# Kernel optimization log

Measured on AMD Instinct MI355X. Metric: run time of the kernel, lower is better.

## Reference

```python
import jax, jax.numpy as jnp
import numpy as np

K, B, D, H = 8, 8192, 1024, 256


def setup_inputs() -> dict:
    key = jax.random.key(0)
    k_x, k_w1, k_w2 = jax.random.split(key, 3)
    x = jax.random.normal(k_x, (B, D), dtype=jnp.float32)
    # He-ish scaled weights so reconstructions stay finite
    W1 = jax.random.normal(k_w1, (K, D, H), dtype=jnp.float32) * (1.0 / np.sqrt(D))
    b1 = jnp.zeros((K, H), dtype=jnp.float32)
    W2 = jax.random.normal(k_w2, (K, H, D), dtype=jnp.float32) * (1.0 / np.sqrt(H))
    b2 = jnp.zeros((K, D), dtype=jnp.float32)
    return {"x": x, "W1": W1, "b1": b1, "W2": W2, "b2": b2}


def reference(x, W1, b1, W2, b2):
    # Run every expert AE on the full batch (matches predict()):
    h = jax.nn.relu(jnp.einsum('bd,kdh->kbh', x, W1) + b1[:, None, :])   # [K,B,H]
    recon = jnp.einsum('kbh,khd->kbd', h, W2) + b2[:, None, :]            # [K,B,D]
    # per-sample reconstruction MSE per expert
    err = jnp.mean((recon - x[None]) ** 2, axis=-1)                       # [K,B]
    # cluster_assignment = argmax over (-err) == argmin over err
    assign = jnp.argmin(err, axis=0)                                      # [B] int
    # gather-compute-scatter: select the winning expert's reconstruction
    x_out = recon[assign, jnp.arange(recon.shape[1])]                     # [B,D]
    return x_out
```

## Files before the change

### kernel.cpp

```cpp
#include <hip/hip_runtime.h>


#define KE 8
#define NB 8192
#define ND 1024
#define NH 256

typedef float f32x4 __attribute__((ext_vector_type(4)));
typedef short s16x8 __attribute__((ext_vector_type(8)));
typedef unsigned short u16x8 __attribute__((ext_vector_type(8)));

__device__ __forceinline__ float bf2f(unsigned short h) {
  union { unsigned int u; float f; } v; v.u = ((unsigned int)h) << 16; return v.f;
}
__device__ __forceinline__ unsigned short f2bf(float f) {
  union { unsigned int u; float f; } v; v.f = f;
  unsigned int u = v.u;
  u += 0x7fffu + ((u >> 16) & 1u);
  return (unsigned short)(u >> 16);
}
__device__ __forceinline__ void split2(float x, unsigned short& hi, unsigned short& lo) {
  hi = f2bf(x);
  lo = f2bf(x - bf2f(hi));
}

__global__ __launch_bounds__(256) void pack_all(
    const float* __restrict__ W1, unsigned short* __restrict__ w1oh, unsigned short* __restrict__ w1ol,
    const float* __restrict__ W2, unsigned short* __restrict__ w2oh, unsigned short* __restrict__ w2ol,
    const float* __restrict__ xin, unsigned short* __restrict__ xoh, unsigned short* __restrict__ xol,
    unsigned int* __restrict__ cnt) {
  const int bx = blockIdx.x;
  const int tid = threadIdx.x;
  if (bx == 0 && tid < KE) cnt[tid] = 0;

  if (bx < 1024) {
    int gid = bx * 256 + tid;
    int L = gid & 63;
    int g = gid >> 6;
    int ks = g & 31;
    int ct = (g >> 5) & 15;
    int k = g >> 9;
    int col = ct * 16 + (L & 15);
    int kd0 = ks * 32 + (L >> 4) * 8;
    unsigned short th[8], tl[8];
#pragma unroll
    for (int j = 0; j < 8; ++j) {
      float v = W1[((size_t)k * ND + kd0 + j) * NH + col];
      split2(v, th[j], tl[j]);
    }
    size_t o = ((size_t)g * 64 + L) * 8;
    *(u16x8*)&w1oh[o] = *(u16x8*)th;
    *(u16x8*)&w1ol[o] = *(u16x8*)tl;
  } else if (bx < 2048) {
    int gid = (bx - 1024) * 256 + tid;
    int L = gid & 63;
    int g = gid >> 6;
    int ks = g & 7;
    int dt = (g >> 3) & 63;
    int k = g >> 9;
    int d2 = dt * 16 + (L & 15);
    int h0 = ks * 32 + (L >> 4) * 8;
    unsigned short th[8], tl[8];
#pragma unroll
    for (int j = 0; j < 8; ++j) {
      float v = W2[((size_t)k * NH + h0 + j) * ND + d2];
      split2(v, th[j], tl[j]);
    }
    size_t o = ((size_t)g * 64 + L) * 8;
    *(u16x8*)&w2oh[o] = *(u16x8*)th;
    *(u16x8*)&w2ol[o] = *(u16x8*)tl;
  } else {
    int gid = (bx - 2048) * 256 + tid;
    int L = gid & 63;
    int g = gid >> 6;
    int ks = g & 31;
    int rt = g >> 5;
    int row = rt * 16 + (L & 15);
    int kd0 = ks * 32 + (L >> 4) * 8;
    float4 a = *(const float4*)&xin[(size_t)row * ND + kd0];
    float4 b = *(const float4*)&xin[(size_t)row * ND + kd0 + 4];
    unsigned short th[8], tl[8];
    split2(a.x, th[0], tl[0]); split2(a.y, th[1], tl[1]);
    split2(a.z, th[2], tl[2]); split2(a.w, th[3], tl[3]);
    split2(b.x, th[4], tl[4]); split2(b.y, th[5], tl[5]);
    split2(b.z, th[6], tl[6]); split2(b.w, th[7], tl[7]);
    size_t o = ((size_t)g * 64 + L) * 8;
    *(u16x8*)&xoh[o] = *(u16x8*)th;
    *(u16x8*)&xol[o] = *(u16x8*)tl;
  }
}

#define LOAD_STAGE(ah, al, bh, bl, it)                  \
  do {                                                  \
    _Pragma("unroll")                                   \
    for (int q_ = 0; q_ < 4; ++q_) {                    \
      int o_ = xo[q_] + (it) * 512;                     \
      ah[q_] = *(const s16x8*)&xph[o_];                 \
      al[q_] = *(const s16x8*)&xpl[o_];                 \
    }                                                   \
    _Pragma("unroll")                                   \
    for (int q_ = 0; q_ < 4; ++q_) {                    \
      int o_ = wo1[q_] + (it) * 512;                    \
      bh[q_] = *(const s16x8*)&w1ph[o_];                \
      bl[q_] = *(const s16x8*)&w1pl[o_];                \
    }                                                   \
  } while (0)

#define MFMA_STAGE(ah, al, bh, bl)                                                                   \
  do {                                                                                               \
    _Pragma("unroll")                                                                                \
    for (int nt_ = 0; nt_ < 4; ++nt_)                                                                \
      _Pragma("unroll")                                                                              \
      for (int mt_ = 0; mt_ < 4; ++mt_) {                                                            \
        acc1[mt_][nt_] = __builtin_amdgcn_mfma_f32_16x16x32_bf16(ah[mt_], bh[nt_], acc1[mt_][nt_], 0, 0, 0); \
        acc1[mt_][nt_] = __builtin_amdgcn_mfma_f32_16x16x32_bf16(ah[mt_], bl[nt_], acc1[mt_][nt_], 0, 0, 0); \
        acc1[mt_][nt_] = __builtin_amdgcn_mfma_f32_16x16x32_bf16(al[mt_], bh[nt_], acc1[mt_][nt_], 0, 0, 0); \
      }                                                                                              \
  } while (0)

__global__ __launch_bounds__(256, 2) void ae_pass1(
    const unsigned short* __restrict__ xph, const unsigned short* __restrict__ xpl,
    const float* __restrict__ x,
    const unsigned short* __restrict__ w1ph, const unsigned short* __restrict__ w1pl,
    const float* __restrict__ b1,
    const unsigned short* __restrict__ w2ph, const unsigned short* __restrict__ w2pl,
    const float* __restrict__ b2, float* __restrict__ err) {
  __shared__ union {
    struct { unsigned short h[64][256]; unsigned short l[64][256]; } hs;
    float errp[4][64];
  } s;

  const int tid = threadIdx.x;
  const int wv = tid >> 6;
  const int lane = tid & 63;
  const int lo = lane & 15;
  const int quad = lane >> 4;
  const int k = (blockIdx.x >> 3) & 7;
  const int rtile = (int)(((blockIdx.x >> 6) << 3) | (blockIdx.x & 7));
  const int r0 = rtile * 64;

  int xo[4], wo1[4];
#pragma unroll
  for (int mt = 0; mt < 4; ++mt) xo[mt] = ((rtile * 4 + mt) * 32) * 512 + lane * 8;
#pragma unroll
  for (int nt = 0; nt < 4; ++nt) wo1[nt] = ((k * 16 + wv * 4 + nt) * 32) * 512 + lane * 8;

  f32x4 acc1[4][4];
#pragma unroll
  for (int mt = 0; mt < 4; ++mt)
#pragma unroll
    for (int nt = 0; nt < 4; ++nt) acc1[mt][nt] = (f32x4){0.f, 0.f, 0.f, 0.f};

  s16x8 Aah[4], Aal[4], Abh[4], Abl[4];
  s16x8 Bah[4], Bal[4], Bbh[4], Bbl[4];
  LOAD_STAGE(Aah, Aal, Abh, Abl, 0);
  LOAD_STAGE(Bah, Bal, Bbh, Bbl, 1);
  for (int it = 0; it < 32; it += 2) {
    MFMA_STAGE(Aah, Aal, Abh, Abl);
    if (it + 2 < 32) LOAD_STAGE(Aah, Aal, Abh, Abl, it + 2);
    MFMA_STAGE(Bah, Bal, Bbh, Bbl);
    if (it + 3 < 32) LOAD_STAGE(Bah, Bal, Bbh, Bbl, it + 3);
  }

#pragma unroll
  for (int nt = 0; nt < 4; ++nt) {
    float b1v = b1[(size_t)k * NH + wv * 64 + nt * 16 + lo];
#pragma unroll
    for (int mt = 0; mt < 4; ++mt)
#pragma unroll
      for (int i = 0; i < 4; ++i) {
        float v = acc1[mt][nt][i] + b1v;
        v = v > 0.f ? v : 0.f;
        unsigned short vh, vl;
        split2(v, vh, vl);
        int row = mt * 16 + quad * 4 + i, col = wv * 64 + nt * 16 + lo;
        int sc = col ^ ((row & 7) << 3);
        s.hs.h[row][sc] = vh;
        s.hs.l[row][sc] = vl;
      }
  }
  __syncthreads();

  float eacc[4][4];
#pragma unroll
  for (int mt = 0; mt < 4; ++mt)
#pragma unroll
    for (int i = 0; i < 4; ++i) eacc[mt][i] = 0.f;

  const int w2base = ((k * 64 + wv * 16) * 8) * 512 + lane * 8;

  for (int mc = 0; mc < 2; ++mc) {
    s16x8 hh[2][8], hl[2][8];
#pragma unroll
    for (int m2 = 0; m2 < 2; ++m2) {
      int row = (mc * 2 + m2) * 16 + lo;
      int rbase = row * 256;
      int sw = (row & 7) << 3;
#pragma unroll
      for (int ks = 0; ks < 8; ++ks) {
        int off = rbase + ((ks * 32 + quad * 8) ^ sw);
        hh[m2][ks] = *(const s16x8*)(&s.hs.h[0][0] + off);
        hl[m2][ks] = *(const s16x8*)(&s.hs.l[0][0] + off);
      }
    }
    for (int dt = 0; dt < 16; ++dt) {
      f32x4 acc2[2];
      acc2[0] = (f32x4){0.f, 0.f, 0.f, 0.f};
      acc2[1] = (f32x4){0.f, 0.f, 0.f, 0.f};
#pragma unroll
      for (int ks = 0; ks < 8; ++ks) {
        int wo = w2base + dt * 4096 + ks * 512;
        s16x8 bh = *(const s16x8*)&w2ph[wo];
        s16x8 bl = *(const s16x8*)&w2pl[wo];
#pragma unroll
        for (int m2 = 0; m2 < 2; ++m2) {
          acc2[m2] = __builtin_amdgcn_mfma_f32_16x16x32_bf16(hh[m2][ks], bh, acc2[m2], 0, 0, 0);
          acc2[m2] = __builtin_amdgcn_mfma_f32_16x16x32_bf16(hh[m2][ks], bl, acc2[m2], 0, 0, 0);
          acc2[m2] = __builtin_amdgcn_mfma_f32_16x16x32_bf16(hl[m2][ks], bh, acc2[m2], 0, 0, 0);
        }
      }
      const int d2 = wv * 256 + dt * 16 + lo;
      float b2v = b2[(size_t)k * ND + d2];
#pragma unroll
      for (int m2 = 0; m2 < 2; ++m2)
#pragma unroll
        for (int i = 0; i < 4; ++i) {
          int row = (mc * 2 + m2) * 16 + quad * 4 + i;
          float rec = acc2[m2][i] + b2v;
          float xv = x[(size_t)(r0 + row) * ND + d2];
          float dd = rec - xv;
          eacc[mc * 2 + m2][i] += dd * dd;
        }
    }
  }

  __syncthreads();
#pragma unroll
  for (int mt = 0; mt < 4; ++mt)
#pragma unroll
    for (int i = 0; i < 4; ++i) {
      float v = eacc[mt][i];
      v += __shfl_xor(v, 1, 16);
      v += __shfl_xor(v, 2, 16);
      v += __shfl_xor(v, 4, 16);
      v += __shfl_xor(v, 8, 16);
      if (lo == 0) s.errp[wv][mt * 16 + quad * 4 + i] = v;
    }
  __syncthreads();
  if (tid < 64)
    err[(size_t)k * NB + r0 + tid] =
        (s.errp[0][tid] + s.errp[1][tid] + s.errp[2][tid] + s.errp[3][tid]) * (1.0f / (float)ND);
}

__global__ __launch_bounds__(256) void ae_argmin(const float* __restrict__ err,
                                                 unsigned int* __restrict__ cnt,
                                                 int* __restrict__ bucket) {
  __shared__ unsigned int lc[KE];
  __shared__ unsigned int base[KE];
  int tid = threadIdx.x;
  if (tid < KE) lc[tid] = 0;
  __syncthreads();
  int b = blockIdx.x * 256 + tid;
  float best = err[b];
  int kmin = 0;
#pragma unroll
  for (int j = 1; j < KE; ++j) {
    float e = err[(size_t)j * NB + b];
    if (e < best) { best = e; kmin = j; }
  }
  unsigned int lpos = atomicAdd(&lc[kmin], 1u);
  __syncthreads();
  if (tid < KE) base[tid] = atomicAdd(&cnt[tid], lc[tid]);
  __syncthreads();
  bucket[(size_t)kmin * NB + (int)(base[kmin] + lpos)] = b;
}

__global__ __launch_bounds__(256) void ae_pass2(
    const float* __restrict__ x,
    const unsigned short* __restrict__ w1ph, const float* __restrict__ b1,
    const unsigned short* __restrict__ w2ph, const float* __restrict__ b2,
    const unsigned int* __restrict__ cnt, const int* __restrict__ bucket,
    float* __restrict__ out) {
  __shared__ unsigned short hs[64][NH + 8];
  __shared__ unsigned short xs[64][40];
  __shared__ int rid[64];

  const int k = blockIdx.x & 7;
  const int cv = (int)cnt[k];
  const int t0 = (blockIdx.x >> 3) * 64;
  if (t0 >= cv) return;
  const int nrows = min(64, cv - t0);

  const int tid = threadIdx.x;
  const int wv = tid >> 6;
  const int lane = tid & 63;
  const int lo = lane & 15;
  const int quad = lane >> 4;
  const int srow = tid >> 2, scol = (tid & 3) * 8;

  if (tid < 64) {
    int idx = t0 + tid;
    rid[tid] = bucket[(size_t)k * NB + (idx < cv ? idx : t0)];
  }
  __syncthreads();
  const int grow = rid[srow];

  f32x4 acc1[4][4];
#pragma unroll
  for (int mt = 0; mt < 4; ++mt)
#pragma unroll
    for (int nt = 0; nt < 4; ++nt) acc1[mt][nt] = (f32x4){0.f, 0.f, 0.f, 0.f};

  for (int it = 0; it < 32; ++it) {
    float4 xa = *(const float4*)&x[(size_t)grow * ND + it * 32 + scol];
    float4 xb = *(const float4*)&x[(size_t)grow * ND + it * 32 + scol + 4];
    s16x8 bfr[4];
#pragma unroll
    for (int nt = 0; nt < 4; ++nt)
      bfr[nt] = *(const s16x8*)&w1ph[(((size_t)(k * 16 + wv * 4 + nt) * 32) + it) * 512 + lane * 8];
    __syncthreads();
    unsigned short t[8];
    t[0] = f2bf(xa.x); t[1] = f2bf(xa.y); t[2] = f2bf(xa.z); t[3] = f2bf(xa.w);
    t[4] = f2bf(xb.x); t[5] = f2bf(xb.y); t[6] = f2bf(xb.z); t[7] = f2bf(xb.w);
    *(u16x8*)&xs[srow][scol] = *(u16x8*)t;
    __syncthreads();
    s16x8 af[4];
#pragma unroll
    for (int mt = 0; mt < 4; ++mt) af[mt] = *(const s16x8*)&xs[mt * 16 + lo][quad * 8];
#pragma unroll
    for (int mt = 0; mt < 4; ++mt)
#pragma unroll
      for (int nt = 0; nt < 4; ++nt)
        acc1[mt][nt] = __builtin_amdgcn_mfma_f32_16x16x32_bf16(af[mt], bfr[nt], acc1[mt][nt], 0, 0, 0);
  }
  __syncthreads();

#pragma unroll
  for (int nt = 0; nt < 4; ++nt) {
    float b1v = b1[(size_t)k * NH + wv * 64 + nt * 16 + lo];
#pragma unroll
    for (int mt = 0; mt < 4; ++mt)
#pragma unroll
      for (int i = 0; i < 4; ++i) {
        float v = acc1[mt][nt][i] + b1v;
        v = v > 0.f ? v : 0.f;
        hs[mt * 16 + quad * 4 + i][wv * 64 + nt * 16 + lo] = f2bf(v);
      }
  }
  __syncthreads();

  for (int c = 0; c < 32; ++c) {
    f32x4 acc2[2];
    acc2[0] = (f32x4){0.f, 0.f, 0.f, 0.f};
    acc2[1] = (f32x4){0.f, 0.f, 0.f, 0.f};
#pragma unroll
    for (int ks = 0; ks < 8; ++ks) {
      s16x8 af = *(const s16x8*)&hs[wv * 16 + lo][ks * 32 + quad * 8];
#pragma unroll
      for (int nt = 0; nt < 2; ++nt) {
        s16x8 bfr = *(const s16x8*)&w2ph[(((size_t)(k * 64 + c * 2 + nt) * 8) + ks) * 512 + lane * 8];
        acc2[nt] = __builtin_amdgcn_mfma_f32_16x16x32_bf16(af, bfr, acc2[nt], 0, 0, 0);
      }
    }
#pragma unroll
    for (int nt = 0; nt < 2; ++nt) {
      float b2v = b2[(size_t)k * ND + c * 32 + nt * 16 + lo];
#pragma unroll
      for (int i = 0; i < 4; ++i) {
        int row = wv * 16 + quad * 4 + i;
        if (row < nrows)
          out[(size_t)rid[row] * ND + c * 32 + nt * 16 + lo] = acc2[nt][i] + b2v;
      }
    }
  }
}

extern "C" void kernel_launch(void* const* d_in, const int* in_sizes, int n_in,
                              void* d_out, int out_size, void* d_ws, size_t ws_size,
                              hipStream_t stream) {
  (void)in_sizes; (void)n_in; (void)out_size; (void)ws_size;
  const float* x  = (const float*)d_in[0];
  const float* W1 = (const float*)d_in[1];
  const float* b1 = (const float*)d_in[2];
  const float* W2 = (const float*)d_in[3];
  const float* b2 = (const float*)d_in[4];
  float* out = (float*)d_out;

  char* ws = (char*)d_ws;
  const size_t szW = (size_t)KE * ND * NH * sizeof(unsigned short);
  const size_t szX = (size_t)NB * ND * sizeof(unsigned short);
  unsigned short* w1ph = (unsigned short*)(ws);
  unsigned short* w1pl = (unsigned short*)(ws + szW);
  unsigned short* w2ph = (unsigned short*)(ws + 2 * szW);
  unsigned short* w2pl = (unsigned short*)(ws + 3 * szW);
  unsigned short* xph  = (unsigned short*)(ws + 4 * szW);
  unsigned short* xpl  = (unsigned short*)(ws + 4 * szW + szX);
  char* tail           = ws + 4 * szW + 2 * szX;
  float* err           = (float*)tail;
  int* bucket          = (int*)(tail + (size_t)KE * NB * sizeof(float));
  unsigned int* cnt    = (unsigned int*)(tail + (size_t)KE * NB * sizeof(float)
                                         + (size_t)KE * NB * sizeof(int));

  pack_all<<<6144, 256, 0, stream>>>(W1, w1ph, w1pl, W2, w2ph, w2pl, x, xph, xpl, cnt);
  ae_pass1<<<1024, 256, 0, stream>>>(xph, xpl, x, w1ph, w1pl, b1, w2ph, w2pl, b2, err);
  ae_argmin<<<NB / 256, 256, 0, stream>>>(err, cnt, bucket);
  ae_pass2<<<1024, 256, 0, stream>>>(x, w1ph, b1, w2ph, b2, cnt, bucket, out);
}
```

Measured before the change: 422.4 us.

## Cache layer-1 hidden activations from pass1 to skip recompute in pass2

Pass1 now writes the bf16 hi part of the ReLU hidden activations for every expert and row into workspace. A new pass2 kernel gathers the winning expert's hidden row from that buffer and only runs the second GEMM, instead of recomputing x·W1. This trades the layer-1 recompute in pass2 for 32 MB of extra global writes in pass1 and gathered reads in pass2. The fast path is taken only if the workspace is large enough; otherwise the old kernel runs.

```diff
diff --git a/kernel.cpp b/kernel.cpp
--- a/kernel.cpp
+++ b/kernel.cpp
@@ -124,7 +124,8 @@
     const unsigned short* __restrict__ w1ph, const unsigned short* __restrict__ w1pl,
     const float* __restrict__ b1,
     const unsigned short* __restrict__ w2ph, const unsigned short* __restrict__ w2pl,
-    const float* __restrict__ b2, float* __restrict__ err) {
+    const float* __restrict__ b2, float* __restrict__ err,
+    unsigned short* __restrict__ hglob) {
   __shared__ union {
     struct { unsigned short h[64][256]; unsigned short l[64][256]; } hs;
     float errp[4][64];
@@ -162,6 +163,7 @@
     if (it + 3 < 32) LOAD_STAGE(Bah, Bal, Bbh, Bbl, it + 3);
   }
 
+  const bool wh = (hglob != nullptr);
 #pragma unroll
   for (int nt = 0; nt < 4; ++nt) {
     float b1v = b1[(size_t)k * NH + wv * 64 + nt * 16 + lo];
@@ -177,6 +179,7 @@
         int sc = col ^ ((row & 7) << 3);
         s.hs.h[row][sc] = vh;
         s.hs.l[row][sc] = vl;
+        if (wh) hglob[((size_t)k * NB + r0 + row) * NH + col] = vh;
       }
   }
   __syncthreads();
@@ -273,6 +276,63 @@
   if (tid < KE) base[tid] = atomicAdd(&cnt[tid], lc[tid]);
   __syncthreads();
   bucket[(size_t)kmin * NB + (int)(base[kmin] + lpos)] = b;
+}
+
+__global__ __launch_bounds__(256) void ae_pass2_fast(
+    const unsigned short* __restrict__ hglob,
+    const unsigned short* __restrict__ w2ph, const float* __restrict__ b2,
+    const unsigned int* __restrict__ cnt, const int* __restrict__ bucket,
+    float* __restrict__ out) {
+  __shared__ int rid[64];
+
+  const int k = blockIdx.x & 7;
+  const int cv = (int)cnt[k];
+  const int t0 = (blockIdx.x >> 3) * 64;
+  if (t0 >= cv) return;
+  const int nrows = min(64, cv - t0);
+
+  const int tid = threadIdx.x;
+  const int wv = tid >> 6;
+  const int lane = tid & 63;
+  const int lo = lane & 15;
+  const int quad = lane >> 4;
+
+  if (tid < 64) {
+    int idx = t0 + tid;
+    rid[tid] = bucket[(size_t)k * NB + (idx < cv ? idx : t0)];
+  }
+  __syncthreads();
+
+  const int grow = rid[wv * 16 + lo];
+  s16x8 af[8];
+  const size_t hbase = ((size_t)k * NB + grow) * NH + quad * 8;
+#pragma unroll
+  for (int ks = 0; ks < 8; ++ks)
+    af[ks] = *(const s16x8*)&hglob[hbase + ks * 32];
+
+  for (int c = 0; c < 32; ++c) {
+    f32x4 acc2[2];
+    acc2[0] = (f32x4){0.f, 0.f, 0.f, 0.f};
+    acc2[1] = (f32x4){0.f, 0.f, 0.f, 0.f};
+#pragma unroll
+    for (int ks = 0; ks < 8; ++ks) {
+#pragma unroll
+      for (int nt = 0; nt < 2; ++nt) {
+        s16x8 bfr = *(const s16x8*)&w2ph[(((size_t)(k * 64 + c * 2 + nt) * 8) + ks) * 512 + lane * 8];
+        acc2[nt] = __builtin_amdgcn_mfma_f32_16x16x32_bf16(af[ks], bfr, acc2[nt], 0, 0, 0);
+      }
+    }
+#pragma unroll
+    for (int nt = 0; nt < 2; ++nt) {
+      float b2v = b2[(size_t)k * ND + c * 32 + nt * 16 + lo];
+#pragma unroll
+      for (int i = 0; i < 4; ++i) {
+        int row = wv * 16 + quad * 4 + i;
+        if (row < nrows)
+          out[(size_t)rid[row] * ND + c * 32 + nt * 16 + lo] = acc2[nt][i] + b2v;
+      }
+    }
+  }
 }
 
 __global__ __launch_bounds__(256) void ae_pass2(
@@ -378,7 +438,7 @@
 extern "C" void kernel_launch(void* const* d_in, const int* in_sizes, int n_in,
                               void* d_out, int out_size, void* d_ws, size_t ws_size,
                               hipStream_t stream) {
-  (void)in_sizes; (void)n_in; (void)out_size; (void)ws_size;
+  (void)in_sizes; (void)n_in; (void)out_size;
   const float* x  = (const float*)d_in[0];
   const float* W1 = (const float*)d_in[1];
   const float* b1 = (const float*)d_in[2];
@@ -400,9 +460,16 @@
   int* bucket          = (int*)(tail + (size_t)KE * NB * sizeof(float));
   unsigned int* cnt    = (unsigned int*)(tail + (size_t)KE * NB * sizeof(float)
                                          + (size_t)KE * NB * sizeof(int));
+  size_t base = 4 * szW + 2 * szX + (size_t)KE * NB * (sizeof(float) + sizeof(int)) + 4096;
+  size_t hbytes = (size_t)KE * NB * NH * sizeof(unsigned short);
+  unsigned short* hglob = (ws_size >= base + hbytes)
+                              ? (unsigned short*)(ws + base) : nullptr;
 
   pack_all<<<6144, 256, 0, stream>>>(W1, w1ph, w1pl, W2, w2ph, w2pl, x, xph, xpl, cnt);
-  ae_pass1<<<1024, 256, 0, stream>>>(xph, xpl, x, w1ph, w1pl, b1, w2ph, w2pl, b2, err);
+  ae_pass1<<<1024, 256, 0, stream>>>(xph, xpl, x, w1ph, w1pl, b1, w2ph, w2pl, b2, err, hglob);
   ae_argmin<<<NB / 256, 256, 0, stream>>>(err, cnt, bucket);
-  ae_pass2<<<1024, 256, 0, stream>>>(x, w1ph, b1, w2ph, b2, cnt, bucket, out);
-}
+  if (hglob)
+    ae_pass2_fast<<<1024, 256, 0, stream>>>(hglob, w2ph, b2, cnt, bucket, out);
+  else
+    ae_pass2<<<1024, 256, 0, stream>>>(x, w1ph, b1, w2ph, b2, cnt, bucket, out);
+}
```

New measurement: 407.4 us. -3.5%, faster.
